# Kernel tuning notes

Measured on AMD Instinct MI355X. Metric: run time of the kernel, lower is better.

## Reference

```python
import jax, jax.numpy as jnp
import numpy as np

H = 16      # num_head
D = 1024    # feat_dim
DK = D // H # per-head dim
B, S = 2, 2048


def setup_inputs() -> dict:
    key = jax.random.key(0)
    ks = jax.random.split(key, 11)
    scale = 1.0 / np.sqrt(D)
    inp = {
        'query': jax.random.normal(ks[0], (B, S, D), jnp.float32),
        'key':   jax.random.normal(ks[1], (B, S, D), jnp.float32),
        'value': jax.random.normal(ks[2], (B, S, D), jnp.float32),
        # causal lower-triangular mask (seq, seq); 0 entries get -1e9
        'mask':  jnp.tril(jnp.ones((S, S), jnp.int32)),
        # torch nn.Linear params: y = x @ W.T + b
        'w_q': jax.random.normal(ks[3], (D, D), jnp.float32) * scale,
        'b_q': jax.random.normal(ks[4], (D,), jnp.float32) * scale,
        'w_k': jax.random.normal(ks[5], (D, D), jnp.float32) * scale,
        'b_k': jax.random.normal(ks[6], (D,), jnp.float32) * scale,
        'w_v': jax.random.normal(ks[7], (D, D), jnp.float32) * scale,
        'b_v': jax.random.normal(ks[8], (D,), jnp.float32) * scale,
        'w_out': jax.random.normal(ks[9], (D, D), jnp.float32) * scale,
        'b_out': jax.random.normal(ks[10], (D,), jnp.float32) * scale,
    }
    return inp


def reference(query, key, value, mask, w_q, b_q, w_k, b_k, w_v, b_v, w_out, b_out):
    b = query.shape[0]
    # projections + split heads -> (b, h, s, d_k)
    def proj(x, w, bias):
        y = x @ w.T + bias
        return y.reshape(b, -1, H, DK).transpose(0, 2, 1, 3)
    q = proj(query, w_q, b_q)
    k = proj(key, w_k, b_k)
    v = proj(value, w_v, b_v)
    # scaled dot-product attention with materialized score matrix
    scores = jnp.einsum('bhqd,bhkd->bhqk', q, k) / np.sqrt(DK).astype(jnp.float32)
    scores = jnp.where(mask == 0, jnp.float32(-1e9), scores)
    attn = jax.nn.softmax(scores, axis=-1)  # dropout is identity in eval mode
    x = jnp.einsum('bhqk,bhkd->bhqd', attn, v)
    x = x.transpose(0, 2, 1, 3).reshape(b, -1, H * DK)
    return x @ w_out.T + b_out
```

## Files before the change

kernel.cpp:

```cpp
#include <hip/hip_runtime.h>

typedef unsigned short u16;
typedef __attribute__((ext_vector_type(8))) short short8;
typedef __attribute__((ext_vector_type(8))) unsigned short u16x8;
typedef __attribute__((ext_vector_type(4))) float floatx4;
typedef __attribute__((ext_vector_type(16))) float floatx16;

#define S2LOG 0.18033688f

__device__ __forceinline__ u16 f2bf(float f) {
    unsigned int u = __float_as_uint(f);
    return (u16)((u + 0x7FFFu + ((u >> 16) & 1u)) >> 16);
}
__device__ __forceinline__ u16 f2bf_hu(float f) {
    return (u16)((__float_as_uint(f) + 0x8000u) >> 16);
}
__device__ __forceinline__ void gl_lds16(const u16* g, u16* l) {
    __builtin_amdgcn_global_load_lds(
        (const __attribute__((address_space(1))) void*)g,
        (__attribute__((address_space(3))) void*)l, 16, 0, 0);
}

__global__ __launch_bounds__(256) void cvt_all(
    const float* __restrict__ q, const float* __restrict__ k, const float* __restrict__ v,
    const float* __restrict__ wq, const float* __restrict__ wk,
    const float* __restrict__ wv, const float* __restrict__ wo,
    u16* __restrict__ ws)
{
    const int b = blockIdx.x, t = threadIdx.x;
    const float* src; u16* dst; long blk;
    if      (b < 2048) { src = q;  dst = ws;            blk = b; }
    else if (b < 4096) { src = k;  dst = ws + 4194304;  blk = b - 2048; }
    else if (b < 6144) { src = v;  dst = ws + 8388608;  blk = b - 4096; }
    else if (b < 6656) { src = wq; dst = ws + 12582912; blk = b - 6144; }
    else if (b < 7168) { src = wk; dst = ws + 13631488; blk = b - 6656; }
    else if (b < 7680) { src = wv; dst = ws + 14680064; blk = b - 7168; }
    else               { src = wo; dst = ws + 15728640; blk = b - 7680; }
    const long i = blk * 2048 + (long)t * 8;
    const float4 a = *(const float4*)(src + i);
    const float4 c = *(const float4*)(src + i + 4);
    u16x8 o;
    o[0] = f2bf(a.x); o[1] = f2bf(a.y); o[2] = f2bf(a.z); o[3] = f2bf(a.w);
    o[4] = f2bf(c.x); o[5] = f2bf(c.y); o[6] = f2bf(c.z); o[7] = f2bf(c.w);
    *(u16x8*)(dst + i) = o;
}

__device__ __forceinline__ void gemm_core64(
    const u16* __restrict__ A, const u16* __restrict__ Bw,
    int m0, int n0, floatx4 (&acc)[2][4])
{
    __shared__ u16 As[2][128 * 64];
    __shared__ u16 Bs[2][64 * 64];
    const int t = threadIdx.x, w = t >> 6;
    const int lane = t & 63, col = lane & 15, quad = lane >> 4;
    const int c7 = col & 7;

#pragma unroll
    for (int i = 0; i < 2; ++i)
#pragma unroll
        for (int j = 0; j < 4; ++j) acc[i][j] = (floatx4)0.f;

    auto stage = [&](int k0, int buf) {
#pragma unroll
        for (int jj = 0; jj < 4; ++jj) {
            const int c = jj * 256 + t;
            const int row = c >> 3, kc = (c & 7) ^ (row & 7);
            gl_lds16(A + (size_t)(m0 + row) * 1024 + k0 + kc * 8,
                     As[buf] + (jj * 256 + w * 64) * 8);
        }
#pragma unroll
        for (int jj = 0; jj < 2; ++jj) {
            const int c = jj * 256 + t;
            const int row = c >> 3, kc = (c & 7) ^ (row & 7);
            gl_lds16(Bw + (size_t)(n0 + row) * 1024 + k0 + kc * 8,
                     Bs[buf] + (jj * 256 + w * 64) * 8);
        }
    };

    stage(0, 0);
    int cur = 0;
    for (int k0 = 0; k0 < 1024; k0 += 64) {
        asm volatile("s_waitcnt vmcnt(0)" ::: "memory");
        __builtin_amdgcn_s_barrier();
        if (k0 + 64 < 1024) stage(k0 + 64, cur ^ 1);
#pragma unroll
        for (int ks = 0; ks < 2; ++ks) {
            const int swz = (ks * 4 + quad) ^ c7;
            short8 af[2], bf[4];
#pragma unroll
            for (int i = 0; i < 2; ++i)
                af[i] = *(const short8*)&As[cur][((w * 32 + i * 16 + col) * 8 + swz) * 8];
#pragma unroll
            for (int j = 0; j < 4; ++j)
                bf[j] = *(const short8*)&Bs[cur][((j * 16 + col) * 8 + swz) * 8];
#pragma unroll
            for (int i = 0; i < 2; ++i)
#pragma unroll
                for (int j = 0; j < 4; ++j)
                    acc[i][j] = __builtin_amdgcn_mfma_f32_16x16x32_bf16(
                        af[i], bf[j], acc[i][j], 0, 0, 0);
        }
        asm volatile("s_waitcnt lgkmcnt(0)" ::: "memory");
        cur ^= 1;
    }
}

__device__ __forceinline__ void gemm_core128(
    const u16* __restrict__ A, const u16* __restrict__ Bw,
    int m0, int n0, floatx4 (&acc)[4][4])
{
    __shared__ u16 As[2][128 * 32];
    __shared__ u16 Bs[2][128 * 32];
    const int t = threadIdx.x, w = t >> 6;
    const int lane = t & 63, col = lane & 15, quad = lane >> 4;
    const int wr = (w >> 1) * 64, wc = (w & 1) * 64;
    const int swz = quad ^ (col & 3) ^ ((col >> 2) & 3);

#pragma unroll
    for (int i = 0; i < 4; ++i)
#pragma unroll
        for (int j = 0; j < 4; ++j) acc[i][j] = (floatx4)0.f;

    auto stage = [&](int k0, int buf) {
#pragma unroll
        for (int jj = 0; jj < 2; ++jj) {
            const int c = jj * 256 + t;
            const int row = c >> 2;
            const int kc = (c & 3) ^ (row & 3) ^ ((row >> 2) & 3);
            gl_lds16(A + (size_t)(m0 + row) * 1024 + k0 + kc * 8,
                     As[buf] + (jj * 256 + w * 64) * 8);
            gl_lds16(Bw + (size_t)(n0 + row) * 1024 + k0 + kc * 8,
                     Bs[buf] + (jj * 256 + w * 64) * 8);
        }
    };

    stage(0, 0);
    int cur = 0;
    for (int k0 = 0; k0 < 1024; k0 += 32) {
        asm volatile("s_waitcnt vmcnt(0)" ::: "memory");
        __builtin_amdgcn_s_barrier();
        if (k0 + 32 < 1024) stage(k0 + 32, cur ^ 1);
        short8 af[4], bf[4];
#pragma unroll
        for (int i = 0; i < 4; ++i)
            af[i] = *(const short8*)&As[cur][((wr + i * 16 + col) * 4 + swz) * 8];
#pragma unroll
        for (int j = 0; j < 4; ++j)
            bf[j] = *(const short8*)&Bs[cur][((wc + j * 16 + col) * 4 + swz) * 8];
        __builtin_amdgcn_s_setprio(1);
#pragma unroll
        for (int i = 0; i < 4; ++i)
#pragma unroll
            for (int j = 0; j < 4; ++j)
                acc[i][j] = __builtin_amdgcn_mfma_f32_16x16x32_bf16(
                    af[i], bf[j], acc[i][j], 0, 0, 0);
        __builtin_amdgcn_s_setprio(0);
        asm volatile("s_waitcnt lgkmcnt(0)" ::: "memory");
        cur ^= 1;
    }
}

__global__ __launch_bounds__(256) void gemm_qkv(
    const u16* __restrict__ xq, const u16* __restrict__ xk, const u16* __restrict__ xv,
    const u16* __restrict__ wqb, const u16* __restrict__ wkb, const u16* __restrict__ wvb,
    const float* __restrict__ bq, const float* __restrict__ bk, const float* __restrict__ bv,
    u16* __restrict__ Qh, u16* __restrict__ Kh, u16* __restrict__ Vt)
{
    const int z = blockIdx.z;
    const u16*   A    = z == 0 ? xq  : z == 1 ? xk  : xv;
    const u16*   Bw   = z == 0 ? wqb : z == 1 ? wkb : wvb;
    const float* bias = z == 0 ? bq  : z == 1 ? bk  : bv;
    u16*         out  = z == 0 ? Qh  : z == 1 ? Kh  : Vt;
    const float  scale = z == 0 ? S2LOG : 1.0f;
    const int m0 = blockIdx.x * 128, n0 = blockIdx.y * 128;

    floatx4 acc[4][4];
    gemm_core128(A, Bw, m0, n0, acc);

    const int t = threadIdx.x, w = t >> 6;
    const int lane = t & 63, col = lane & 15, quad = lane >> 4;
    const int wr = (w >> 1) * 64, wc = (w & 1) * 64;
#pragma unroll
    for (int i = 0; i < 4; ++i)
#pragma unroll
        for (int j = 0; j < 4; ++j)
#pragma unroll
            for (int reg = 0; reg < 4; ++reg) {
                const int gm = m0 + wr + i * 16 + quad * 4 + reg;
                const int gn = n0 + wc + j * 16 + col;
                const float val = (acc[i][j][reg] + bias[gn]) * scale;
                const int bb = gm >> 11, ss = gm & 2047, hh = gn >> 6, dd = gn & 63;
                if (z != 2)
                    out[(((size_t)bb * 16 + hh) * 2048 + ss) * 64 + dd] = f2bf(val);
                else
                    out[(((size_t)bb * 16 + hh) * 64 + dd) * 2048 + ss] = f2bf(val);
            }
}

__global__ __launch_bounds__(256) void gemm_out(
    const u16* __restrict__ A, const u16* __restrict__ Bw,
    const float* __restrict__ bias, float* __restrict__ out)
{
    const int m0 = blockIdx.x * 128, n0 = blockIdx.y * 64;
    floatx4 acc[2][4];
    gemm_core64(A, Bw, m0, n0, acc);
    const int t = threadIdx.x, w = t >> 6;
    const int lane = t & 63, col = lane & 15, quad = lane >> 4;
#pragma unroll
    for (int i = 0; i < 2; ++i)
#pragma unroll
        for (int j = 0; j < 4; ++j)
#pragma unroll
            for (int reg = 0; reg < 4; ++reg) {
                const int gm = m0 + w * 32 + i * 16 + quad * 4 + reg;
                const int gn = n0 + j * 16 + col;
                out[(size_t)gm * 1024 + gn] = acc[i][j][reg] + bias[gn];
            }
}

__global__ __launch_bounds__(256) void attn_mfma(
    const u16* __restrict__ Qh, const u16* __restrict__ Kh,
    const u16* __restrict__ Vt, u16* __restrict__ ctx)
{
    __shared__ u16 QPs[128 * 64];
    __shared__ u16 Ks[2][64 * 64];
    __shared__ u16 Vs[2][64 * 64];
    const int t = threadIdx.x, w = t >> 6;
    const int lane = t & 63;
    const int col = lane & 31;
    const int hi  = lane >> 5;
    const int l7  = lane & 7;
    const int bh = blockIdx.y;
    const int qt = (bh < 16) ? (15 - (int)blockIdx.x) : (int)blockIdx.x;
    const int q0 = qt * 128;
    const u16* qg = Qh + ((size_t)bh * 2048 + q0) * 64;
    const u16* kg = Kh + (size_t)bh * 2048 * 64;
    const u16* vg = Vt + (size_t)bh * 2048 * 64;

    auto stage = [&](int tile, int buf) {
#pragma unroll
        for (int jj = 0; jj < 2; ++jj) {
            const int c = jj * 256 + t;
            const int row = c >> 3, kc = (c & 7) ^ (row & 7);
            gl_lds16(kg + (size_t)(tile * 64 + row) * 64 + kc * 8,
                     Ks[buf] + (jj * 256 + w * 64) * 8);
            gl_lds16(vg + (size_t)row * 2048 + tile * 64 + kc * 8,
                     Vs[buf] + (jj * 256 + w * 64) * 8);
        }
    };

#pragma unroll
    for (int jj = 0; jj < 4; ++jj) {
        const int c = jj * 256 + t;
        const int row = c >> 3, kc = (c & 7) ^ (row & 7);
        gl_lds16(qg + (size_t)row * 64 + kc * 8, QPs + (jj * 256 + w * 64) * 8);
    }
    stage(0, 0);
    asm volatile("s_waitcnt vmcnt(4)" ::: "memory");
    __builtin_amdgcn_s_barrier();

    short8 qf[4];
#pragma unroll
    for (int tq = 0; tq < 4; ++tq)
        qf[tq] = *(const short8*)
            &QPs[((w * 32 + col) * 8 + ((2 * tq + hi) ^ l7)) * 8];

    floatx16 oacc[2];
    oacc[0] = (floatx16)0.f; oacc[1] = (floatx16)0.f;
    float ls = 0.f;
    const int qrow = q0 + w * 32 + col;

    const int ktmax = 2 * qt + 1;
    int cur = 0;
    for (int kt = 0; kt <= ktmax; ++kt) {
        asm volatile("s_waitcnt vmcnt(0)" ::: "memory");
        __builtin_amdgcn_s_barrier();
        if (kt + 1 <= ktmax) stage(kt + 1, cur ^ 1);
        const bool pm = (kt >= 2 * qt);

#pragma unroll
        for (int sub = 0; sub < 2; ++sub) {
            const int krow = sub * 32 + col;
            short8 kf[4];
#pragma unroll
            for (int tq = 0; tq < 4; ++tq)
                kf[tq] = *(const short8*)
                    &Ks[cur][(krow * 8 + ((2 * tq + hi) ^ l7)) * 8];

            floatx16 sacc = (floatx16)0.f;
#pragma unroll
            for (int tq = 0; tq < 4; ++tq)
                sacc = __builtin_amdgcn_mfma_f32_32x32x16_bf16(
                    kf[tq], qf[tq], sacc, 0, 0, 0);

            u16 ph[16];
#pragma unroll
            for (int r = 0; r < 16; ++r) {
                float pe = __builtin_amdgcn_exp2f(sacc[r]);
                u16 h = f2bf_hu(pe);
                if (pm && (kt * 64 + sub * 32 + (r & 3) + 8 * (r >> 2) + 4 * hi > qrow))
                    h = 0;
                ph[r] = h;
                ls += __uint_as_float((unsigned)h << 16);
            }

            short8 pa[2];
#pragma unroll
            for (int s = 0; s < 2; ++s) {
                unsigned A0 = (unsigned)ph[8 * s + 0] | ((unsigned)ph[8 * s + 1] << 16);
                unsigned A1 = (unsigned)ph[8 * s + 2] | ((unsigned)ph[8 * s + 3] << 16);
                unsigned B0 = (unsigned)ph[8 * s + 4] | ((unsigned)ph[8 * s + 5] << 16);
                unsigned B1 = (unsigned)ph[8 * s + 6] | ((unsigned)ph[8 * s + 7] << 16);
                asm("v_permlane32_swap_b32 %0, %1" : "+v"(A0), "+v"(B0));
                asm("v_permlane32_swap_b32 %0, %1" : "+v"(A1), "+v"(B1));
                union { unsigned u[4]; short8 s8; } cv;
                cv.u[0] = A0; cv.u[1] = A1; cv.u[2] = B0; cv.u[3] = B1;
                pa[s] = cv.s8;
            }

#pragma unroll
            for (int dt = 0; dt < 2; ++dt) {
                const int vrow = dt * 32 + col;
#pragma unroll
                for (int s = 0; s < 2; ++s) {
                    const int ksv = sub * 2 + s;
                    short8 vf = *(const short8*)
                        &Vs[cur][(vrow * 8 + ((2 * ksv + hi) ^ l7)) * 8];
                    oacc[dt] = __builtin_amdgcn_mfma_f32_32x32x16_bf16(
                        pa[s], vf, oacc[dt], 0, 0, 0);
                }
            }
        }
        cur ^= 1;
    }

    const float lt = ls + __shfl_xor(ls, 32);
    const int bb = bh >> 4, hh = bh & 15;
#pragma unroll
    for (int reg = 0; reg < 16; ++reg) {
        const int qr = (reg & 3) + 8 * (reg >> 2) + 4 * hi;
        const float lq = __shfl(lt, qr, 64);
        const float inv = __builtin_amdgcn_rcpf(lq);
        const int qrs = q0 + w * 32 + qr;
#pragma unroll
        for (int dt = 0; dt < 2; ++dt)
            ctx[((size_t)bb * 2048 + qrs) * 1024 + hh * 64 + dt * 32 + col] =
                f2bf(oacc[dt][reg] * inv);
    }
}

extern "C" void kernel_launch(void* const* d_in, const int* in_sizes, int n_in,
                              void* d_out, int out_size, void* d_ws, size_t ws_size,
                              hipStream_t stream)
{
    const float* query = (const float*)d_in[0];
    const float* key   = (const float*)d_in[1];
    const float* value = (const float*)d_in[2];
    const float* w_q   = (const float*)d_in[4];
    const float* b_q   = (const float*)d_in[5];
    const float* w_k   = (const float*)d_in[6];
    const float* b_k   = (const float*)d_in[7];
    const float* w_v   = (const float*)d_in[8];
    const float* b_v   = (const float*)d_in[9];
    const float* w_out = (const float*)d_in[10];
    const float* b_out = (const float*)d_in[11];

    u16* W = (u16*)d_ws;
    u16* xq  = W;
    u16* xk  = W + 4194304;
    u16* xv  = W + 8388608;
    u16* wqb = W + 12582912;
    u16* wkb = W + 13631488;
    u16* wvb = W + 14680064;
    u16* wob = W + 15728640;
    u16* Qh  = W + 16777216;
    u16* Kh  = W + 20971520;
    u16* Vtw = W + 25165824;
    u16* ctx = W + 29360128;

    hipLaunchKernelGGL(cvt_all, dim3(8192), dim3(256), 0, stream,
                       query, key, value, w_q, w_k, w_v, w_out, W);

    hipLaunchKernelGGL(gemm_qkv, dim3(32, 8, 3), dim3(256), 0, stream,
                       xq, xk, xv, wqb, wkb, wvb, b_q, b_k, b_v, Qh, Kh, Vtw);

    hipLaunchKernelGGL(attn_mfma, dim3(16, 32), dim3(256), 0, stream, Qh, Kh, Vtw, ctx);

    hipLaunchKernelGGL(gemm_out, dim3(32, 16), dim3(256), 0, stream,
                       ctx, wob, b_out, (float*)d_out);
}
```

Measured before the change: 242.3 us.

## Store attention tiles in MFMA fragment order and use packed bf16 conversion

Shared-memory tiles for Q, K and V are rearranged so that each 512-element chunk holds exactly one MFMA operand fragment. A lane then reads its fragment with a contiguous lane*8 offset instead of going through an XOR swizzle. Probability values are kept in float, masking only runs on diagonal tiles, and pairs are converted with v_cvt_pk_bf16_f32 in place of manual rounding and packing. The row sum now accumulates unrounded float probabilities, which differ slightly from the bf16 values fed to the MFMA. The global load pattern also changes and may coalesce less well.

```diff
diff --git a/kernel.cpp b/kernel.cpp
--- a/kernel.cpp
+++ b/kernel.cpp
@@ -11,9 +11,6 @@
 __device__ __forceinline__ u16 f2bf(float f) {
     unsigned int u = __float_as_uint(f);
     return (u16)((u + 0x7FFFu + ((u >> 16) & 1u)) >> 16);
-}
-__device__ __forceinline__ u16 f2bf_hu(float f) {
-    return (u16)((__float_as_uint(f) + 0x8000u) >> 16);
 }
 __device__ __forceinline__ void gl_lds16(const u16* g, u16* l) {
     __builtin_amdgcn_global_load_lds(
@@ -222,14 +219,13 @@
     const u16* __restrict__ Qh, const u16* __restrict__ Kh,
     const u16* __restrict__ Vt, u16* __restrict__ ctx)
 {
-    __shared__ u16 QPs[128 * 64];
-    __shared__ u16 Ks[2][64 * 64];
-    __shared__ u16 Vs[2][64 * 64];
+    __shared__ u16 Qs[16 * 512];
+    __shared__ u16 Ks[2][8 * 512];
+    __shared__ u16 Vs[2][8 * 512];
     const int t = threadIdx.x, w = t >> 6;
     const int lane = t & 63;
     const int col = lane & 31;
     const int hi  = lane >> 5;
-    const int l7  = lane & 7;
     const int bh = blockIdx.y;
     const int qt = (bh < 16) ? (15 - (int)blockIdx.x) : (int)blockIdx.x;
     const int q0 = qt * 128;
@@ -240,20 +236,19 @@
     auto stage = [&](int tile, int buf) {
 #pragma unroll
         for (int jj = 0; jj < 2; ++jj) {
-            const int c = jj * 256 + t;
-            const int row = c >> 3, kc = (c & 7) ^ (row & 7);
-            gl_lds16(kg + (size_t)(tile * 64 + row) * 64 + kc * 8,
-                     Ks[buf] + (jj * 256 + w * 64) * 8);
-            gl_lds16(vg + (size_t)row * 2048 + tile * 64 + kc * 8,
-                     Vs[buf] + (jj * 256 + w * 64) * 8);
+            const int cidx = jj * 4 + w;
+            gl_lds16(kg + (size_t)(tile * 64 + jj * 32 + col) * 64 + w * 16 + hi * 8,
+                     Ks[buf] + cidx * 512);
+            gl_lds16(vg + (size_t)(jj * 32 + col) * 2048 + tile * 64 + w * 16 + hi * 8,
+                     Vs[buf] + cidx * 512);
         }
     };
 
 #pragma unroll
     for (int jj = 0; jj < 4; ++jj) {
-        const int c = jj * 256 + t;
-        const int row = c >> 3, kc = (c & 7) ^ (row & 7);
-        gl_lds16(qg + (size_t)row * 64 + kc * 8, QPs + (jj * 256 + w * 64) * 8);
+        const int cidx = jj * 4 + w;
+        gl_lds16(qg + (size_t)(jj * 32 + col) * 64 + w * 16 + hi * 8,
+                 Qs + cidx * 512);
     }
     stage(0, 0);
     asm volatile("s_waitcnt vmcnt(4)" ::: "memory");
@@ -262,8 +257,7 @@
     short8 qf[4];
 #pragma unroll
     for (int tq = 0; tq < 4; ++tq)
-        qf[tq] = *(const short8*)
-            &QPs[((w * 32 + col) * 8 + ((2 * tq + hi) ^ l7)) * 8];
+        qf[tq] = *(const short8*)&Qs[(w * 4 + tq) * 512 + lane * 8];
 
     floatx16 oacc[2];
     oacc[0] = (floatx16)0.f; oacc[1] = (floatx16)0.f;
@@ -280,12 +274,10 @@
 
 #pragma unroll
         for (int sub = 0; sub < 2; ++sub) {
-            const int krow = sub * 32 + col;
             short8 kf[4];
 #pragma unroll
             for (int tq = 0; tq < 4; ++tq)
-                kf[tq] = *(const short8*)
-                    &Ks[cur][(krow * 8 + ((2 * tq + hi) ^ l7)) * 8];
+                kf[tq] = *(const short8*)&Ks[cur][(sub * 4 + tq) * 512 + lane * 8];
 
             floatx16 sacc = (floatx16)0.f;
 #pragma unroll
@@ -293,24 +285,29 @@
                 sacc = __builtin_amdgcn_mfma_f32_32x32x16_bf16(
                     kf[tq], qf[tq], sacc, 0, 0, 0);
 
-            u16 ph[16];
-#pragma unroll
-            for (int r = 0; r < 16; ++r) {
-                float pe = __builtin_amdgcn_exp2f(sacc[r]);
-                u16 h = f2bf_hu(pe);
-                if (pm && (kt * 64 + sub * 32 + (r & 3) + 8 * (r >> 2) + 4 * hi > qrow))
-                    h = 0;
-                ph[r] = h;
-                ls += __uint_as_float((unsigned)h << 16);
+            float pe[16];
+#pragma unroll
+            for (int r = 0; r < 16; ++r)
+                pe[r] = __builtin_amdgcn_exp2f(sacc[r]);
+            if (pm) {
+                const int kbase = kt * 64 + sub * 32;
+#pragma unroll
+                for (int r = 0; r < 16; ++r) {
+                    const int rkv = (r & 3) + 8 * (r >> 2) + 4 * hi;
+                    if (kbase + rkv > qrow) pe[r] = 0.f;
+                }
             }
+#pragma unroll
+            for (int r = 0; r < 16; ++r) ls += pe[r];
 
             short8 pa[2];
 #pragma unroll
             for (int s = 0; s < 2; ++s) {
-                unsigned A0 = (unsigned)ph[8 * s + 0] | ((unsigned)ph[8 * s + 1] << 16);
-                unsigned A1 = (unsigned)ph[8 * s + 2] | ((unsigned)ph[8 * s + 3] << 16);
-                unsigned B0 = (unsigned)ph[8 * s + 4] | ((unsigned)ph[8 * s + 5] << 16);
-                unsigned B1 = (unsigned)ph[8 * s + 6] | ((unsigned)ph[8 * s + 7] << 16);
+                unsigned A0, A1, B0, B1;
+                asm("v_cvt_pk_bf16_f32 %0, %1, %2" : "=v"(A0) : "v"(pe[8*s+0]), "v"(pe[8*s+1]));
+                asm("v_cvt_pk_bf16_f32 %0, %1, %2" : "=v"(A1) : "v"(pe[8*s+2]), "v"(pe[8*s+3]));
+                asm("v_cvt_pk_bf16_f32 %0, %1, %2" : "=v"(B0) : "v"(pe[8*s+4]), "v"(pe[8*s+5]));
+                asm("v_cvt_pk_bf16_f32 %0, %1, %2" : "=v"(B1) : "v"(pe[8*s+6]), "v"(pe[8*s+7]));
                 asm("v_permlane32_swap_b32 %0, %1" : "+v"(A0), "+v"(B0));
                 asm("v_permlane32_swap_b32 %0, %1" : "+v"(A1), "+v"(B1));
                 union { unsigned u[4]; short8 s8; } cv;
@@ -319,17 +316,14 @@
             }
 
 #pragma unroll
-            for (int dt = 0; dt < 2; ++dt) {
-                const int vrow = dt * 32 + col;
+            for (int dt = 0; dt < 2; ++dt)
 #pragma unroll
                 for (int s = 0; s < 2; ++s) {
-                    const int ksv = sub * 2 + s;
                     short8 vf = *(const short8*)
-                        &Vs[cur][(vrow * 8 + ((2 * ksv + hi) ^ l7)) * 8];
+                        &Vs[cur][(dt * 4 + sub * 2 + s) * 512 + lane * 8];
                     oacc[dt] = __builtin_amdgcn_mfma_f32_32x32x16_bf16(
                         pa[s], vf, oacc[dt], 0, 0, 0);
                 }
-            }
         }
         cur ^= 1;
     }
```

Result: faster. 234.6 us (-3.2%).
